# Kernel optimization log

Hardware: AMD Instinct MI355X
Metric: run time of the kernel (lower is better)

Reference implementation:

```python
import jax, jax.numpy as jnp
import numpy as np

B, S, D = 1, 2048, 4096
H, KVH, DH = 32, 8, 128
NEG_INF = jnp.finfo(jnp.float32).min


def rotate_half(x):
    x1, x2 = jnp.split(x, 2, axis=-1)
    return jnp.concatenate([-x2, x1], axis=-1)


def setup_inputs() -> dict:
    key = jax.random.key(0)
    ks = jax.random.split(key, 6)
    hidden_states = jax.random.normal(ks[0], (B, S, D), dtype=jnp.float32)
    # proper llama RoPE tables
    inv_freq = 1.0 / (10000.0 ** (jnp.arange(0, DH, 2, dtype=jnp.float32) / DH))
    pos = jnp.arange(S, dtype=jnp.float32)
    freqs = pos[:, None] * inv_freq[None, :]            # [S, DH/2]
    emb = jnp.concatenate([freqs, freqs], axis=-1)       # [S, DH]
    cos = jnp.cos(emb)
    sin = jnp.sin(emb)
    # additive causal mask [B,1,S,S]
    causal = jnp.tril(jnp.ones((S, S), dtype=bool))
    attention_mask = jnp.where(causal, 0.0, NEG_INF)[None, None].astype(jnp.float32)
    sc = 0.02
    Wq = jax.random.normal(ks[1], (D, H * DH), dtype=jnp.float32) * sc
    Wk = jax.random.normal(ks[2], (D, KVH * DH), dtype=jnp.float32) * sc
    Wv = jax.random.normal(ks[3], (D, KVH * DH), dtype=jnp.float32) * sc
    Wo = jax.random.normal(ks[4], (H * DH, D), dtype=jnp.float32) * sc
    return {"hidden_states": hidden_states, "cos": cos, "sin": sin,
            "attention_mask": attention_mask, "Wq": Wq, "Wk": Wk, "Wv": Wv, "Wo": Wo}


def reference(hidden_states, cos, sin, attention_mask, Wq, Wk, Wv, Wo):
    b, s, _ = hidden_states.shape
    scaling = DH ** -0.5
    q = (hidden_states @ Wq).reshape(b, s, H, DH).transpose(0, 2, 1, 3)     # [B,H,S,DH]
    k = (hidden_states @ Wk).reshape(b, s, KVH, DH).transpose(0, 2, 1, 3)   # [B,KVH,S,DH]
    v = (hidden_states @ Wv).reshape(b, s, KVH, DH).transpose(0, 2, 1, 3)
    c = cos[None, None]  # [1,1,S,DH]
    sn = sin[None, None]
    q = q * c + rotate_half(q) * sn
    k = k * c + rotate_half(k) * sn
    n_rep = H // KVH
    k = jnp.repeat(k, n_rep, axis=1)  # [B,H,S,DH]
    v = jnp.repeat(v, n_rep, axis=1)
    scores = jnp.einsum('bhqd,bhkd->bhqk', q, k) * scaling
    scores = jnp.maximum(scores + attention_mask, NEG_INF)
    probs = jax.nn.softmax(scores.astype(jnp.float32), axis=-1).astype(q.dtype)
    attn = jnp.einsum('bhqk,bhkd->bhqd', probs, v)
    attn = attn.transpose(0, 2, 1, 3).reshape(b, s, H * DH)
    return attn @ Wo
```

## Files before the change

kernel.cpp:

```cpp
#include <hip/hip_runtime.h>
#include <hip/hip_bf16.h>
#include <stdint.h>

typedef unsigned short u16;
typedef unsigned int u32;
typedef __bf16 bf16x8 __attribute__((ext_vector_type(8)));
typedef float f32x4 __attribute__((ext_vector_type(4)));
typedef u16 u16x8 __attribute__((ext_vector_type(8)));

#define S_LEN 2048
#define DMODEL 4096
#define NHEADS 32
#define NKVH 8
#define DHEAD 128
#define LDQK 6144

__device__ __forceinline__ float bf2f(u16 x) {
    union { u32 i; float f; } u; u.i = ((u32)x) << 16; return u.f;
}
__device__ __forceinline__ u16 f2bf(float f) {
    union { float f; u32 i; } u; u.f = f;
    u32 x = u.i;
    return (u16)((x + 0x7fffu + ((x >> 16) & 1u)) >> 16);
}
__device__ __forceinline__ bf16x8 ld_bf8(const void* p) {
    int4 v = *(const int4*)p;
    return __builtin_bit_cast(bf16x8, v);
}

__global__ void k_cvt(const float* __restrict__ in, u16* __restrict__ out, int n8) {
    int i = blockIdx.x * 256 + threadIdx.x;
    if (i >= n8) return;
    const float4* p = (const float4*)in + (size_t)i * 2;
    float4 a = p[0], b = p[1];
    u16x8 o;
    o[0]=f2bf(a.x); o[1]=f2bf(a.y); o[2]=f2bf(a.z); o[3]=f2bf(a.w);
    o[4]=f2bf(b.x); o[5]=f2bf(b.y); o[6]=f2bf(b.z); o[7]=f2bf(b.w);
    *((u16x8*)out + i) = o;
}

template<typename TIN>
__global__ void k_transpose_bf16(const TIN* __restrict__ in, u16* __restrict__ out,
                                 int R, int C, int ldin) {
    __shared__ u16 tile[32][33];
    int c0 = blockIdx.x * 32, r0 = blockIdx.y * 32;
    int tx = threadIdx.x & 31, ty = threadIdx.x >> 5;
    #pragma unroll
    for (int i = 0; i < 4; i++) {
        int r = ty + i * 8;
        TIN v = in[(size_t)(r0 + r) * ldin + c0 + tx];
        if constexpr (sizeof(TIN) == 4) tile[r][tx] = f2bf((float)v);
        else tile[r][tx] = (u16)v;
    }
    __syncthreads();
    #pragma unroll
    for (int i = 0; i < 4; i++) {
        int r = ty + i * 8;
        out[(size_t)(c0 + r) * R + r0 + tx] = tile[tx][r];
    }
}

__global__ void k_rope(u16* __restrict__ X, const float* __restrict__ cosT,
                       const float* __restrict__ sinT, int nh, int ld) {
    int idx = blockIdx.x * 256 + threadIdx.x;
    int d = idx & 63;
    int h = (idx >> 6) % nh;
    int s = idx / (64 * nh);
    u16* p = X + (size_t)s * ld + h * DHEAD;
    float x1 = bf2f(p[d]), x2 = bf2f(p[d + 64]);
    float c1 = cosT[s * DHEAD + d],      s1 = sinT[s * DHEAD + d];
    float c2 = cosT[s * DHEAD + d + 64], s2 = sinT[s * DHEAD + d + 64];
    p[d]      = f2bf(x1 * c1 - x2 * s1);
    p[d + 64] = f2bf(x2 * c2 + x1 * s2);
}

typedef const __attribute__((address_space(1))) u32 GBUF;
typedef __attribute__((address_space(3))) u32 LBUF;

template<typename OUT_T>
__global__ __launch_bounds__(256)
void k_gemm_bt2(const u16* __restrict__ A, const u16* __restrict__ Bt,
                OUT_T* __restrict__ C, int M, int N, int K) {
    __shared__ __align__(16) u16 As[128 * 64];
    __shared__ __align__(16) u16 Bs[128 * 64];
    const int m0 = blockIdx.y * 128, n0 = blockIdx.x * 128;
    const int tid = threadIdx.x, lane = tid & 63, wid = tid >> 6;
    const int wr = wid >> 1, wc = wid & 1;
    const int g = lane >> 4, lr = lane & 15;

    const u16* sA[4]; const u16* sB[4]; u32 dste[4];
    #pragma unroll
    for (int j = 0; j < 4; j++) {
        int c = j * 256 + tid;
        int row = c >> 3;
        int colsw = (c & 7) ^ (row & 7);
        sA[j] = A  + (size_t)(m0 + row) * K + colsw * 8;
        sB[j] = Bt + (size_t)(n0 + row) * K + colsw * 8;
        dste[j] = (u32)c * 8;
    }
    auto rdoff = [&](int row, int kk) -> u32 {
        return (u32)(row * 128 + ((((kk << 2) + g) ^ (row & 7)) << 4));
    };

    f32x4 acc[4][4] = {};

    for (int k0 = 0; k0 < K; k0 += 64) {
        __syncthreads();
        #pragma unroll
        for (int j = 0; j < 4; j++)
            __builtin_amdgcn_global_load_lds((GBUF*)(sA[j] + k0), (LBUF*)(As + dste[j]), 16, 0, 0);
        #pragma unroll
        for (int j = 0; j < 4; j++)
            __builtin_amdgcn_global_load_lds((GBUF*)(sB[j] + k0), (LBUF*)(Bs + dste[j]), 16, 0, 0);
        __syncthreads();

        bf16x8 af[4][2], bfv[4][2];
        #pragma unroll
        for (int i = 0; i < 4; i++)
            #pragma unroll
            for (int kk = 0; kk < 2; kk++)
                af[i][kk] = ld_bf8((const char*)As + rdoff(wr * 64 + i * 16 + lr, kk));
        #pragma unroll
        for (int n = 0; n < 4; n++)
            #pragma unroll
            for (int kk = 0; kk < 2; kk++)
                bfv[n][kk] = ld_bf8((const char*)Bs + rdoff(wc * 64 + n * 16 + lr, kk));
        #pragma unroll
        for (int i = 0; i < 4; i++)
            #pragma unroll
            for (int n = 0; n < 4; n++)
                #pragma unroll
                for (int kk = 0; kk < 2; kk++)
                    acc[i][n] = __builtin_amdgcn_mfma_f32_16x16x32_bf16(
                        af[i][kk], bfv[n][kk], acc[i][n], 0, 0, 0);
    }
    #pragma unroll
    for (int i = 0; i < 4; i++)
        #pragma unroll
        for (int n = 0; n < 4; n++)
            #pragma unroll
            for (int r = 0; r < 4; r++) {
                int row = m0 + wr * 64 + i * 16 + g * 4 + r;
                int col = n0 + wc * 64 + n * 16 + lr;
                float v = acc[i][n][r];
                if constexpr (sizeof(OUT_T) == 2) C[(size_t)row * N + col] = f2bf(v);
                else                              C[(size_t)row * N + col] = v;
            }
}

__global__ __launch_bounds__(256)
void k_attn2(const u16* __restrict__ Qb, const u16* __restrict__ Kb,
             const u16* __restrict__ VbT, u16* __restrict__ Ab) {
    extern __shared__ __align__(16) char smem[];

    const int p = blockIdx.x, h = blockIdx.y, hk = h >> 2;
    const int tid = threadIdx.x, lane = tid & 63, wid = tid >> 6;
    const int g = lane >> 4, lr = lane & 15;
    const float scale = 0.08838834764831845f;
    const int qtA = p, qtB = 31 - p, nA = qtA + 1;
    const int NIT = 33;

    const int krow_l = lane >> 4, kc16 = lane & 15;
    const int vrow_l = lane >> 3, vc8  = lane & 7;

    u16* PsB = (u16*)(smem + 65536) + wid * 16 * 72;

    auto stage = [&](int buf, int k0) {
        u16* KsD = (u16*)smem + buf * 8192;
        u16* VtD = (u16*)(smem + 32768) + buf * 8192;
        #pragma unroll
        for (int j = 0; j < 4; j++) {
            int rowt = wid * 16 + j * 4 + krow_l;
            int c16  = kc16 ^ (rowt & 7);
            __builtin_amdgcn_global_load_lds(
                (GBUF*)(Kb + (size_t)(k0 + rowt) * LDQK + hk * DHEAD + c16 * 8),
                (LBUF*)(KsD + (wid * 16 + j * 4) * 128), 16, 0, 0);
        }
        #pragma unroll
        for (int j = 0; j < 4; j++) {
            int rowt = wid * 32 + j * 8 + vrow_l;
            int c8   = vc8 ^ (rowt & 7);
            __builtin_amdgcn_global_load_lds(
                (GBUF*)(VbT + (size_t)(hk * DHEAD + rowt) * S_LEN + k0 + c8 * 8),
                (LBUF*)(VtD + (wid * 32 + j * 8) * 64), 16, 0, 0);
        }
    };

    bf16x8 qf[4];
    f32x4 acc[8];
    float m[4], lsum[4];
    int qt = qtA, q0 = qtA * 64;

    stage(0, 0);
    asm volatile("s_waitcnt vmcnt(0)" ::: "memory");
    __builtin_amdgcn_s_barrier();

    for (int i = 0; i < NIT; i++) {
        const int kt = (i < nA) ? i : (i - nA);
        if (i + 1 < NIT) {
            int kt1 = (i + 1 < nA) ? (i + 1) : (i + 1 - nA);
            stage((i + 1) & 1, kt1 * 64);
        }
        if (i == 0 || i == nA) {
            if (i == nA) {
                #pragma unroll
                for (int n = 0; n < 8; n++)
                    #pragma unroll
                    for (int r = 0; r < 4; r++)
                        Ab[(size_t)(q0 + wid * 16 + g * 4 + r) * DMODEL + h * DHEAD + n * 16 + lr]
                            = f2bf(acc[n][r] / lsum[r]);
            }
            qt = (i == 0) ? qtA : qtB;
            q0 = qt * 64;
            const u16* qrow = Qb + (size_t)(q0 + wid * 16 + lr) * LDQK + h * DHEAD;
            #pragma unroll
            for (int c = 0; c < 4; c++) qf[c] = ld_bf8(qrow + c * 32 + g * 8);
            #pragma unroll
            for (int n = 0; n < 8; n++) acc[n] = (f32x4){0.f, 0.f, 0.f, 0.f};
            #pragma unroll
            for (int r = 0; r < 4; r++) { m[r] = -1e30f; lsum[r] = 0.f; }
        }

        const char* KsB = smem + (i & 1) * 16384;
        const char* VtB = smem + 32768 + (i & 1) * 16384;

        f32x4 sf[4];
        __builtin_amdgcn_s_setprio(1);
        #pragma unroll
        for (int st = 0; st < 4; st++) {
            f32x4 s = {0.f, 0.f, 0.f, 0.f};
            #pragma unroll
            for (int c = 0; c < 4; c++) {
                int row = st * 16 + lr;
                int cb = (c * 32 + g * 8) * 2;
                bf16x8 kf = ld_bf8(KsB + row * 256 + (cb ^ ((row & 7) << 4)));
                s = __builtin_amdgcn_mfma_f32_16x16x32_bf16(qf[c], kf, s, 0, 0, 0);
            }
            sf[st] = s;
        }
        __builtin_amdgcn_s_setprio(0);

        if (kt == qt) {
            #pragma unroll
            for (int st = 0; st < 4; st++)
                #pragma unroll
                for (int r = 0; r < 4; r++) {
                    int qg = wid * 16 + g * 4 + r;
                    int kg = st * 16 + lr;
                    sf[st][r] = (kg > qg) ? -1e30f : sf[st][r] * scale;
                }
        } else {
            #pragma unroll
            for (int st = 0; st < 4; st++)
                #pragma unroll
                for (int r = 0; r < 4; r++) sf[st][r] *= scale;
        }

        float corr[4];
        int allskip = 1;
        #pragma unroll
        for (int r = 0; r < 4; r++) {
            float v = fmaxf(fmaxf(sf[0][r], sf[1][r]), fmaxf(sf[2][r], sf[3][r]));
            #pragma unroll
            for (int off = 1; off < 16; off <<= 1) v = fmaxf(v, __shfl_xor(v, off, 64));
            bool sk = (v <= m[r] + 8.0f);
            float mn = sk ? m[r] : v;
            corr[r] = sk ? 1.0f : __expf(m[r] - mn);
            m[r] = mn;
            allskip &= (int)sk;
        }
        float ts[4] = {0.f, 0.f, 0.f, 0.f};
        #pragma unroll
        for (int st = 0; st < 4; st++)
            #pragma unroll
            for (int r = 0; r < 4; r++) {
                float pv = __expf(sf[st][r] - m[r]);
                sf[st][r] = pv;
                ts[r] += pv;
            }
        #pragma unroll
        for (int r = 0; r < 4; r++) {
            #pragma unroll
            for (int off = 1; off < 16; off <<= 1) ts[r] += __shfl_xor(ts[r], off, 64);
            lsum[r] = lsum[r] * corr[r] + ts[r];
        }
        if (!__all(allskip)) {
            #pragma unroll
            for (int n = 0; n < 8; n++)
                #pragma unroll
                for (int r = 0; r < 4; r++) acc[n][r] *= corr[r];
        }

        #pragma unroll
        for (int st = 0; st < 4; st++)
            #pragma unroll
            for (int r = 0; r < 4; r++)
                PsB[(g * 4 + r) * 72 + st * 16 + lr] = f2bf(sf[st][r]);
        asm volatile("s_waitcnt lgkmcnt(0)" ::: "memory");

        __builtin_amdgcn_s_setprio(1);
        #pragma unroll
        for (int c2 = 0; c2 < 2; c2++) {
            bf16x8 pa = ld_bf8(PsB + lr * 72 + c2 * 32 + g * 8);
            #pragma unroll
            for (int n = 0; n < 8; n++) {
                int row = n * 16 + lr;
                int cb = (c2 * 32 + g * 8) * 2;
                bf16x8 vf = ld_bf8(VtB + row * 128 + (cb ^ ((row & 7) << 4)));
                acc[n] = __builtin_amdgcn_mfma_f32_16x16x32_bf16(pa, vf, acc[n], 0, 0, 0);
            }
        }
        __builtin_amdgcn_s_setprio(0);

        asm volatile("s_waitcnt lgkmcnt(0)" ::: "memory");
        __builtin_amdgcn_sched_barrier(0);
        asm volatile("s_waitcnt vmcnt(0)" ::: "memory");
        __builtin_amdgcn_s_barrier();
    }

    #pragma unroll
    for (int n = 0; n < 8; n++)
        #pragma unroll
        for (int r = 0; r < 4; r++)
            Ab[(size_t)(q0 + wid * 16 + g * 4 + r) * DMODEL + h * DHEAD + n * 16 + lr]
                = f2bf(acc[n][r] / lsum[r]);
}

extern "C" void kernel_launch(void* const* d_in, const int* in_sizes, int n_in,
                              void* d_out, int out_size, void* d_ws, size_t ws_size,
                              hipStream_t stream) {
    const float* hidden = (const float*)d_in[0];
    const float* cosT   = (const float*)d_in[1];
    const float* sinT   = (const float*)d_in[2];
    const float* Wq = (const float*)d_in[4];
    const float* Wk = (const float*)d_in[5];
    const float* Wv = (const float*)d_in[6];
    const float* Wo = (const float*)d_in[7];
    float* out = (float*)d_out;
    char* ws = (char*)d_ws;

    u16* Xbf   = (u16*)ws;
    u16* WqkvT = (u16*)(ws + (16u << 20));
    u16* VbT   = (u16*)(ws + (16u << 20));
    u16* WoT   = (u16*)(ws + (64u << 20));
    u16* QKVb  = (u16*)(ws + (96u << 20));
    u16* Ab    = Xbf;

    k_cvt<<<dim3((S_LEN * DMODEL / 8) / 256), 256, 0, stream>>>(hidden, Xbf, S_LEN * DMODEL / 8);
    k_transpose_bf16<float><<<dim3(4096 / 32, 4096 / 32), 256, 0, stream>>>(Wq, WqkvT, 4096, 4096, 4096);
    k_transpose_bf16<float><<<dim3(1024 / 32, 4096 / 32), 256, 0, stream>>>(Wk, WqkvT + (size_t)4096 * 4096, 4096, 1024, 1024);
    k_transpose_bf16<float><<<dim3(1024 / 32, 4096 / 32), 256, 0, stream>>>(Wv, WqkvT + (size_t)5120 * 4096, 4096, 1024, 1024);
    k_transpose_bf16<float><<<dim3(4096 / 32, 4096 / 32), 256, 0, stream>>>(Wo, WoT, 4096, 4096, 4096);

    k_gemm_bt2<u16><<<dim3(6144 / 128, 2048 / 128), 256, 0, stream>>>(Xbf, WqkvT, QKVb, 2048, 6144, 4096);

    k_rope<<<(2048 * 32 * 64) / 256, 256, 0, stream>>>(QKVb, cosT, sinT, 32, LDQK);
    k_rope<<<(2048 * 8 * 64) / 256, 256, 0, stream>>>(QKVb + 4096, cosT, sinT, 8, LDQK);

    k_transpose_bf16<u16><<<dim3(1024 / 32, 2048 / 32), 256, 0, stream>>>(QKVb + 5120, VbT, 2048, 1024, LDQK);

    hipFuncSetAttribute((const void*)k_attn2, hipFuncAttributeMaxDynamicSharedMemorySize, 74752);
    k_attn2<<<dim3(16, 32), 256, 74752, stream>>>(QKVb, QKVb + 4096, VbT, Ab);

    k_gemm_bt2<float><<<dim3(4096 / 128, 2048 / 128), 256, 0, stream>>>(Ab, WoT, out, 2048, 4096, 4096);
}
```

Before: 372.5 us.

## Rewrite attention with 32x32 MFMA, register-resident P, and 128-row query tiles

The attention kernel now uses 32x32x16 MFMA with transposed S = K·Q^T, so each lane owns one query row. This turns the row max and sum reductions into a single cross-half shuffle. P is repacked into MFMA operands through register shuffles instead of a round trip through LDS, which also drops the P scratch buffer and lowers shared memory to 64KB. Each block handles a 128-row query tile with a per-wave causal cutoff. Blocks are ordered so heavy and light tiles are balanced, and launch bounds request 2 blocks per CU. The risks are higher register pressure from the 16-wide accumulators and the loss of the paired-tile balancing inside each block.

After: 368.3 us. About the same (-1.1%).

```diff
diff --git a/kernel.cpp b/kernel.cpp
--- a/kernel.cpp
+++ b/kernel.cpp
@@ -6,6 +6,7 @@
 typedef unsigned int u32;
 typedef __bf16 bf16x8 __attribute__((ext_vector_type(8)));
 typedef float f32x4 __attribute__((ext_vector_type(4)));
+typedef float f32x16 __attribute__((ext_vector_type(16)));
 typedef u16 u16x8 __attribute__((ext_vector_type(8)));
 
 #define S_LEN 2048
@@ -148,22 +149,24 @@
             }
 }
 
-__global__ __launch_bounds__(256)
-void k_attn2(const u16* __restrict__ Qb, const u16* __restrict__ Kb,
+__global__ __launch_bounds__(256, 2)
+void k_attn3(const u16* __restrict__ Qb, const u16* __restrict__ Kb,
              const u16* __restrict__ VbT, u16* __restrict__ Ab) {
     extern __shared__ __align__(16) char smem[];
 
-    const int p = blockIdx.x, h = blockIdx.y, hk = h >> 2;
+    const int bid = blockIdx.x;
+    const int idx = bid & 255;
+    int t = idx & 7; if (bid >> 8) t = 15 - t;
+    const int h = idx >> 3, hk = h >> 2;
     const int tid = threadIdx.x, lane = tid & 63, wid = tid >> 6;
-    const int g = lane >> 4, lr = lane & 15;
+    const int ql = lane & 31, hi = lane >> 5;
     const float scale = 0.08838834764831845f;
-    const int qtA = p, qtB = 31 - p, nA = qtA + 1;
-    const int NIT = 33;
+    const int NIT = 2 * t + 2;
+    const int q0w = 128 * t + 32 * wid;
+    const int qg = q0w + ql;
 
     const int krow_l = lane >> 4, kc16 = lane & 15;
     const int vrow_l = lane >> 3, vc8  = lane & 7;
-
-    u16* PsB = (u16*)(smem + 65536) + wid * 16 * 72;
 
     auto stage = [&](int buf, int k0) {
         u16* KsD = (u16*)smem + buf * 8192;
@@ -186,131 +189,119 @@
         }
     };
 
-    bf16x8 qf[4];
-    f32x4 acc[8];
-    float m[4], lsum[4];
-    int qt = qtA, q0 = qtA * 64;
+    bf16x8 qf[8];
+    {
+        const u16* qrow = Qb + (size_t)qg * LDQK + h * DHEAD;
+        #pragma unroll
+        for (int dc = 0; dc < 8; dc++)
+            qf[dc] = ld_bf8(qrow + dc * 16 + hi * 8);
+    }
+
+    f32x16 acc[4] = {};
+    float m = -1e30f, lsum = 0.f;
+    const int imax = 2 * t + (wid >> 1);
 
     stage(0, 0);
     asm volatile("s_waitcnt vmcnt(0)" ::: "memory");
     __builtin_amdgcn_s_barrier();
 
     for (int i = 0; i < NIT; i++) {
-        const int kt = (i < nA) ? i : (i - nA);
-        if (i + 1 < NIT) {
-            int kt1 = (i + 1 < nA) ? (i + 1) : (i + 1 - nA);
-            stage((i + 1) & 1, kt1 * 64);
+        if (i + 1 < NIT) stage((i + 1) & 1, (i + 1) * 64);
+
+        if (i <= imax) {
+            const char* KsB = smem + (i & 1) * 16384;
+            const char* VtB = smem + 32768 + (i & 1) * 16384;
+
+            f32x16 s0 = {}, s1 = {};
+            __builtin_amdgcn_s_setprio(1);
+            #pragma unroll
+            for (int dc = 0; dc < 8; dc++) {
+                int r0 = ql, r1 = 32 + ql;
+                bf16x8 kf0 = ld_bf8(KsB + r0 * 256 + (((2 * dc + hi) ^ (r0 & 7)) << 4));
+                bf16x8 kf1 = ld_bf8(KsB + r1 * 256 + (((2 * dc + hi) ^ (r1 & 7)) << 4));
+                s0 = __builtin_amdgcn_mfma_f32_32x32x16_bf16(kf0, qf[dc], s0, 0, 0, 0);
+                s1 = __builtin_amdgcn_mfma_f32_32x32x16_bf16(kf1, qf[dc], s1, 0, 0, 0);
+            }
+            __builtin_amdgcn_s_setprio(0);
+
+            float p[2][16];
+            bool diag = (64 * i + 63 > q0w);
+            #pragma unroll
+            for (int r = 0; r < 16; r++) {
+                int kloc = (r & 3) + 8 * (r >> 2) + 4 * hi;
+                float v0 = s0[r] * scale, v1 = s1[r] * scale;
+                if (diag) {
+                    int kg = 64 * i + kloc;
+                    if (kg > qg) v0 = -1e30f;
+                    if (kg + 32 > qg) v1 = -1e30f;
+                }
+                p[0][r] = v0; p[1][r] = v1;
+            }
+
+            float mx = p[0][0];
+            #pragma unroll
+            for (int z = 1; z < 16; z++) mx = fmaxf(mx, p[0][z]);
+            #pragma unroll
+            for (int z = 0; z < 16; z++) mx = fmaxf(mx, p[1][z]);
+            mx = fmaxf(mx, __shfl_xor(mx, 32, 64));
+            bool sk = (mx <= m + 8.0f);
+            float mn = sk ? m : mx;
+            float corr = sk ? 1.0f : __expf(m - mn);
+            m = mn;
+            float ts = 0.f;
+            #pragma unroll
+            for (int g2 = 0; g2 < 2; g2++)
+                #pragma unroll
+                for (int z = 0; z < 16; z++) {
+                    float e = __expf(p[g2][z] - mn);
+                    p[g2][z] = e;
+                    ts += e;
+                }
+            ts += __shfl_xor(ts, 32, 64);
+            lsum = lsum * corr + ts;
+            if (!__all(sk)) {
+                float cq[16];
+                #pragma unroll
+                for (int r = 0; r < 16; r++)
+                    cq[r] = __shfl(corr, (r & 3) + 8 * (r >> 2) + 4 * hi, 64);
+                #pragma unroll
+                for (int db = 0; db < 4; db++)
+                    #pragma unroll
+                    for (int r = 0; r < 16; r++) acc[db][r] *= cq[r];
+            }
+
+            bf16x8 pf[4];
+            #pragma unroll
+            for (int g2 = 0; g2 < 2; g2++) {
+                u32 u[8], sw[8];
+                #pragma unroll
+                for (int z = 0; z < 8; z++)
+                    u[z] = (u32)f2bf(p[g2][2 * z]) | ((u32)f2bf(p[g2][2 * z + 1]) << 16);
+                #pragma unroll
+                for (int z = 0; z < 8; z++) sw[z] = __shfl_xor(u[z], 32, 64);
+                #pragma unroll
+                for (int ksl = 0; ksl < 2; ksl++) {
+                    int4 w4;
+                    if (hi) w4 = make_int4(sw[4 * ksl + 2], sw[4 * ksl + 3],
+                                           u[4 * ksl + 2],  u[4 * ksl + 3]);
+                    else    w4 = make_int4(u[4 * ksl],      u[4 * ksl + 1],
+                                           sw[4 * ksl],     sw[4 * ksl + 1]);
+                    pf[2 * g2 + ksl] = __builtin_bit_cast(bf16x8, w4);
+                }
+            }
+
+            __builtin_amdgcn_s_setprio(1);
+            #pragma unroll
+            for (int db = 0; db < 4; db++) {
+                int row = 32 * db + ql;
+                #pragma unroll
+                for (int ks = 0; ks < 4; ks++) {
+                    bf16x8 vf = ld_bf8(VtB + row * 128 + (((2 * ks + hi) ^ (row & 7)) << 4));
+                    acc[db] = __builtin_amdgcn_mfma_f32_32x32x16_bf16(pf[ks], vf, acc[db], 0, 0, 0);
+                }
+            }
+            __builtin_amdgcn_s_setprio(0);
         }
-        if (i == 0 || i == nA) {
-            if (i == nA) {
-                #pragma unroll
-                for (int n = 0; n < 8; n++)
-                    #pragma unroll
-                    for (int r = 0; r < 4; r++)
-                        Ab[(size_t)(q0 + wid * 16 + g * 4 + r) * DMODEL + h * DHEAD + n * 16 + lr]
-                            = f2bf(acc[n][r] / lsum[r]);
-            }
-            qt = (i == 0) ? qtA : qtB;
-            q0 = qt * 64;
-            const u16* qrow = Qb + (size_t)(q0 + wid * 16 + lr) * LDQK + h * DHEAD;
-            #pragma unroll
-            for (int c = 0; c < 4; c++) qf[c] = ld_bf8(qrow + c * 32 + g * 8);
-            #pragma unroll
-            for (int n = 0; n < 8; n++) acc[n] = (f32x4){0.f, 0.f, 0.f, 0.f};
-            #pragma unroll
-            for (int r = 0; r < 4; r++) { m[r] = -1e30f; lsum[r] = 0.f; }
-        }
-
-        const char* KsB = smem + (i & 1) * 16384;
-        const char* VtB = smem + 32768 + (i & 1) * 16384;
-
-        f32x4 sf[4];
-        __builtin_amdgcn_s_setprio(1);
-        #pragma unroll
-        for (int st = 0; st < 4; st++) {
-            f32x4 s = {0.f, 0.f, 0.f, 0.f};
-            #pragma unroll
-            for (int c = 0; c < 4; c++) {
-                int row = st * 16 + lr;
-                int cb = (c * 32 + g * 8) * 2;
-                bf16x8 kf = ld_bf8(KsB + row * 256 + (cb ^ ((row & 7) << 4)));
-                s = __builtin_amdgcn_mfma_f32_16x16x32_bf16(qf[c], kf, s, 0, 0, 0);
-            }
-            sf[st] = s;
-        }
-        __builtin_amdgcn_s_setprio(0);
-
-        if (kt == qt) {
-            #pragma unroll
-            for (int st = 0; st < 4; st++)
-                #pragma unroll
-                for (int r = 0; r < 4; r++) {
-                    int qg = wid * 16 + g * 4 + r;
-                    int kg = st * 16 + lr;
-                    sf[st][r] = (kg > qg) ? -1e30f : sf[st][r] * scale;
-                }
-        } else {
-            #pragma unroll
-            for (int st = 0; st < 4; st++)
-                #pragma unroll
-                for (int r = 0; r < 4; r++) sf[st][r] *= scale;
-        }
-
-        float corr[4];
-        int allskip = 1;
-        #pragma unroll
-        for (int r = 0; r < 4; r++) {
-            float v = fmaxf(fmaxf(sf[0][r], sf[1][r]), fmaxf(sf[2][r], sf[3][r]));
-            #pragma unroll
-            for (int off = 1; off < 16; off <<= 1) v = fmaxf(v, __shfl_xor(v, off, 64));
-            bool sk = (v <= m[r] + 8.0f);
-            float mn = sk ? m[r] : v;
-            corr[r] = sk ? 1.0f : __expf(m[r] - mn);
-            m[r] = mn;
-            allskip &= (int)sk;
-        }
-        float ts[4] = {0.f, 0.f, 0.f, 0.f};
-        #pragma unroll
-        for (int st = 0; st < 4; st++)
-            #pragma unroll
-            for (int r = 0; r < 4; r++) {
-                float pv = __expf(sf[st][r] - m[r]);
-                sf[st][r] = pv;
-                ts[r] += pv;
-            }
-        #pragma unroll
-        for (int r = 0; r < 4; r++) {
-            #pragma unroll
-            for (int off = 1; off < 16; off <<= 1) ts[r] += __shfl_xor(ts[r], off, 64);
-            lsum[r] = lsum[r] * corr[r] + ts[r];
-        }
-        if (!__all(allskip)) {
-            #pragma unroll
-            for (int n = 0; n < 8; n++)
-                #pragma unroll
-                for (int r = 0; r < 4; r++) acc[n][r] *= corr[r];
-        }
-
-        #pragma unroll
-        for (int st = 0; st < 4; st++)
-            #pragma unroll
-            for (int r = 0; r < 4; r++)
-                PsB[(g * 4 + r) * 72 + st * 16 + lr] = f2bf(sf[st][r]);
-        asm volatile("s_waitcnt lgkmcnt(0)" ::: "memory");
-
-        __builtin_amdgcn_s_setprio(1);
-        #pragma unroll
-        for (int c2 = 0; c2 < 2; c2++) {
-            bf16x8 pa = ld_bf8(PsB + lr * 72 + c2 * 32 + g * 8);
-            #pragma unroll
-            for (int n = 0; n < 8; n++) {
-                int row = n * 16 + lr;
-                int cb = (c2 * 32 + g * 8) * 2;
-                bf16x8 vf = ld_bf8(VtB + row * 128 + (cb ^ ((row & 7) << 4)));
-                acc[n] = __builtin_amdgcn_mfma_f32_16x16x32_bf16(pa, vf, acc[n], 0, 0, 0);
-            }
-        }
-        __builtin_amdgcn_s_setprio(0);
 
         asm volatile("s_waitcnt lgkmcnt(0)" ::: "memory");
         __builtin_amdgcn_sched_barrier(0);
@@ -318,12 +309,18 @@
         __builtin_amdgcn_s_barrier();
     }
 
-    #pragma unroll
-    for (int n = 0; n < 8; n++)
-        #pragma unroll
-        for (int r = 0; r < 4; r++)
-            Ab[(size_t)(q0 + wid * 16 + g * 4 + r) * DMODEL + h * DHEAD + n * 16 + lr]
-                = f2bf(acc[n][r] / lsum[r]);
+    float rinv[16];
+    #pragma unroll
+    for (int r = 0; r < 16; r++)
+        rinv[r] = 1.0f / __shfl(lsum, (r & 3) + 8 * (r >> 2) + 4 * hi, 64);
+    #pragma unroll
+    for (int db = 0; db < 4; db++)
+        #pragma unroll
+        for (int r = 0; r < 16; r++) {
+            int crow = (r & 3) + 8 * (r >> 2) + 4 * hi;
+            Ab[(size_t)(q0w + crow) * DMODEL + h * DHEAD + db * 32 + ql]
+                = f2bf(acc[db][r] * rinv[r]);
+        }
 }
 
 extern "C" void kernel_launch(void* const* d_in, const int* in_sizes, int n_in,
@@ -359,8 +356,8 @@
 
     k_transpose_bf16<u16><<<dim3(1024 / 32, 2048 / 32), 256, 0, stream>>>(QKVb + 5120, VbT, 2048, 1024, LDQK);
 
-    hipFuncSetAttribute((const void*)k_attn2, hipFuncAttributeMaxDynamicSharedMemorySize, 74752);
-    k_attn2<<<dim3(16, 32), 256, 74752, stream>>>(QKVb, QKVb + 4096, VbT, Ab);
+    hipFuncSetAttribute((const void*)k_attn3, hipFuncAttributeMaxDynamicSharedMemorySize, 65536);
+    k_attn3<<<dim3(512), 256, 65536, stream>>>(QKVb, QKVb + 4096, VbT, Ab);
 
     k_gemm_bt2<float><<<dim3(4096 / 128, 2048 / 128), 256, 0, stream>>>(Ab, WoT, out, 2048, 4096, 4096);
 }
```
